# Kernel optimization log

Hardware: AMD Instinct MI355X
Metric: run time of the kernel (lower is better)

Reference implementation:

```python
import jax, jax.numpy as jnp
import numpy as np

B, N, D, H = 2, 2048, 256, 4
DH = D // H  # 64
ALPHA_DIV = 0.01
LN_EPS = 1e-5


def _split_heads(t):
    # [B, N, D] -> [B, H, N, DH]
    b, n, _ = t.shape
    return t.reshape(b, n, H, DH).transpose(0, 2, 1, 3)


def _merge_heads(t):
    # [B, H, N, DH] -> [B, N, D]
    b, h, n, d = t.shape
    return t.transpose(0, 2, 1, 3).reshape(b, n, h * d)


def setup_inputs() -> dict:
    key = jax.random.key(0)
    ks = jax.random.split(key, 20)
    p = lambda k, shape: (jax.random.normal(k, shape, dtype=jnp.float32) * 0.02)
    return {
        "x0": jax.random.normal(ks[0], (B, N, D), dtype=jnp.float32),
        "x1": jax.random.normal(ks[1], (B, N, D), dtype=jnp.float32),
        "cross_mask0": jax.random.uniform(ks[2], (B, 1, N), dtype=jnp.float32),
        "cross_mask1": jax.random.uniform(ks[3], (B, 1, N), dtype=jnp.float32),
        # weights stored as [in, out]
        "Wqk": p(ks[4], (D, D)), "bqk": jnp.zeros((D,), jnp.float32),
        "Wv": p(ks[5], (D, D)), "bv": jnp.zeros((D,), jnp.float32),
        "Wo": p(ks[6], (D, D)), "bo": jnp.zeros((D,), jnp.float32),
        "W1": p(ks[7], (2 * D, 2 * D)), "b1": jnp.zeros((2 * D,), jnp.float32),
        "ln_g": jnp.ones((2 * D,), jnp.float32), "ln_b": jnp.zeros((2 * D,), jnp.float32),
        "W2": p(ks[8], (2 * D, D)), "b2": jnp.zeros((D,), jnp.float32),
    }


def _ffn(x, W1, b1, ln_g, ln_b, W2, b2):
    h = x @ W1 + b1
    mu = jnp.mean(h, -1, keepdims=True)
    var = jnp.var(h, -1, keepdims=True)
    h = (h - mu) * jax.lax.rsqrt(var + LN_EPS) * ln_g + ln_b
    h = jax.nn.gelu(h, approximate=False)
    return h @ W2 + b2


def cross_block(x0, x1, cross_mask0, cross_mask1, Wqk, bqk, Wv, bv, Wo, bo,
                W1, b1, ln_g, ln_b, W2, b2):
    s = (DH ** -0.5) ** 0.5  # scale applied to each of qk0, qk1
    qk0 = _split_heads(x0 @ Wqk + bqk) * s
    qk1 = _split_heads(x1 @ Wqk + bqk) * s
    v0 = _split_heads(x0 @ Wv + bv)
    v1 = _split_heads(x1 @ Wv + bv)

    sim = jnp.einsum('bhid,bhjd->bhij', qk0, qk1)  # [B,H,N0,N1]

    # cross masks: [B,1,N] -> broadcast [B,1,1,N] over heads and query rows
    bad0 = (cross_mask0[:, :, None, :] < ALPHA_DIV)  # masks keys of dir 1->0
    bad1 = (cross_mask1[:, :, None, :] < ALPHA_DIV)  # masks keys of dir 0->1

    attn01 = jax.nn.softmax(jnp.where(bad1, -jnp.inf, sim), axis=-1)             # [B,H,N0,N1]
    attn10 = jax.nn.softmax(jnp.where(bad0, -jnp.inf, sim.swapaxes(-2, -1)), axis=-1)  # [B,H,N1,N0]

    m0 = jnp.einsum('bhij,bhjd->bhid', attn01, v1)
    m1 = jnp.einsum('bhij,bhjd->bhid', attn10, v0)

    m0 = _merge_heads(m0) @ Wo + bo
    m1 = _merge_heads(m1) @ Wo + bo

    out0 = x0 + _ffn(jnp.concatenate([x0, m0], -1), W1, b1, ln_g, ln_b, W2, b2)
    out1 = x1 + _ffn(jnp.concatenate([x1, m1], -1), W1, b1, ln_g, ln_b, W2, b2)
    return out0, out1, attn01, attn10


def reference(x0, x1, cross_mask0, cross_mask1, Wqk, bqk, Wv, bv, Wo, bo,
              W1, b1, ln_g, ln_b, W2, b2):
    return cross_block(x0, x1, cross_mask0, cross_mask1, Wqk, bqk, Wv, bv,
                       Wo, bo, W1, b1, ln_g, ln_b, W2, b2)
```

## Files before the change

### kernel.cpp

```cpp
#include <hip/hip_runtime.h>
#include <hip/hip_bf16.h>
#include <math.h>

#define B 2
#define N 2048
#define D 256
#define H 4
#define DH 64
#define D2 512
#define BH 8
#define BKP 40

static constexpr float ALPHA_DIV = 0.01f;
static constexpr float LN_EPS = 1e-5f;
static constexpr float SCL = 0.35355339059327373f;

typedef __attribute__((ext_vector_type(4))) float f32x4;
typedef __attribute__((ext_vector_type(8))) short s16x8;

__device__ inline s16x8 cvt8_bf16(const float* p) {
    union { s16x8 v; __hip_bfloat16 h[8]; } u;
#pragma unroll
    for (int i = 0; i < 8; i++) u.h[i] = __float2bfloat16(p[i]);
    return u.v;
}

template<int BM, bool OUT_BF16, bool HAS_RES>
__device__ __forceinline__ void gemm_core(
    __hip_bfloat16 (*As)[BKP], __hip_bfloat16 (*Ws)[BKP],
    const __hip_bfloat16* A, int lda, const __hip_bfloat16* WT, int ldw,
    const float* bias, const float* Res, int ldres,
    void* Cvp, int ldc, int K, float alpha, int rowBase, int colBase)
{
    constexpr int WM = BM / 2;
    constexpr int FM = WM / 16;
    constexpr int ACHUNK = (BM * 32) / (256 * 8);

    const int tid = threadIdx.x;
    const int lane = tid & 63, wid = tid >> 6;
    const int wr = wid >> 1, wc = wid & 1;
    const int lr = lane & 15, lk = (lane >> 4) * 8;

    f32x4 acc[FM][2] = {};

    for (int k0 = 0; k0 < K; k0 += 32) {
#pragma unroll
        for (int c = 0; c < ACHUNK; c++) {
            int e = (tid + c * 256) * 8;
            int r = e >> 5, kk = e & 31;
            *(s16x8*)&As[r][kk] = *(const s16x8*)&A[(size_t)(rowBase + r) * lda + k0 + kk];
        }
        {
            int e = tid * 8;
            int n = e >> 5, kk = e & 31;
            *(s16x8*)&Ws[n][kk] = *(const s16x8*)&WT[(size_t)(colBase + n) * ldw + k0 + kk];
        }
        __syncthreads();

        s16x8 a[FM], b[2];
#pragma unroll
        for (int i = 0; i < FM; i++) a[i] = *(const s16x8*)&As[wr * WM + i * 16 + lr][lk];
#pragma unroll
        for (int j = 0; j < 2; j++) b[j] = *(const s16x8*)&Ws[wc * 32 + j * 16 + lr][lk];
#pragma unroll
        for (int i = 0; i < FM; i++)
#pragma unroll
            for (int j = 0; j < 2; j++)
                acc[i][j] = __builtin_amdgcn_mfma_f32_16x16x32_bf16(a[i], b[j], acc[i][j], 0, 0, 0);
        __syncthreads();
    }

#pragma unroll
    for (int i = 0; i < FM; i++) {
#pragma unroll
        for (int j = 0; j < 2; j++) {
            int col = colBase + wc * 32 + j * 16 + lr;
            float bval = bias ? bias[col] : 0.f;
#pragma unroll
            for (int t = 0; t < 4; t++) {
                int row = rowBase + wr * WM + i * 16 + (lane >> 4) * 4 + t;
                float o = alpha * (acc[i][j][t] + bval);
                if (HAS_RES) o += Res[(size_t)row * ldres + col];
                if (OUT_BF16)
                    ((__hip_bfloat16*)Cvp)[(size_t)row * ldc + col] = __float2bfloat16(o);
                else
                    ((float*)Cvp)[(size_t)row * ldc + col] = o;
            }
        }
    }
}

template<bool OUT_BF16, bool HAS_RES>
__global__ __launch_bounds__(256) void gemm128_z(
    const __hip_bfloat16* A0, const __hip_bfloat16* A1, int lda,
    const __hip_bfloat16* WT, int ldw, const float* bias,
    const float* Res0, const float* Res1, int ldres,
    void* C0, void* C1, int ldc, int K, float alpha)
{
    __shared__ __hip_bfloat16 As[128][BKP];
    __shared__ __hip_bfloat16 Ws[64][BKP];
    const __hip_bfloat16* A = blockIdx.z ? A1 : A0;
    const float* Res = blockIdx.z ? Res1 : Res0;
    void* C = blockIdx.z ? C1 : C0;
    gemm_core<128, OUT_BF16, HAS_RES>(As, Ws, A, lda, WT, ldw, bias, Res, ldres,
        C, ldc, K, alpha, blockIdx.y * 128, blockIdx.x * 64);
}

__global__ __launch_bounds__(256) void proj_kernel(
    const float* __restrict__ x0, const float* __restrict__ x1,
    const __hip_bfloat16* __restrict__ WcT, const float* __restrict__ cb,
    __hip_bfloat16* __restrict__ qkv0, __hip_bfloat16* __restrict__ qkv1,
    __hip_bfloat16* __restrict__ vT,
    __hip_bfloat16* __restrict__ xc0, __hip_bfloat16* __restrict__ xc1)
{
    __shared__ __hip_bfloat16 As[128][BKP];
    __shared__ __hip_bfloat16 Ws[64][BKP];
    __shared__ __hip_bfloat16 T[128][72];
    const int z = blockIdx.z;
    const float* x = z ? x1 : x0;
    __hip_bfloat16* qkv = z ? qkv1 : qkv0;
    __hip_bfloat16* xc = z ? xc1 : xc0;
    const int rowBase = blockIdx.y * 128;
    const int colBase = blockIdx.x * 64;
    const int tid = threadIdx.x;
    const int lane = tid & 63, wid = tid >> 6;
    const int wr = wid >> 1, wc = wid & 1;
    const int lr = lane & 15, g = lane >> 4, lk = g * 8;

    f32x4 acc[4][2] = {};
    for (int k0 = 0; k0 < D; k0 += 32) {
#pragma unroll
        for (int c = 0; c < 2; c++) {
            int e = (tid + c * 256) * 8;
            int r = e >> 5, kk = e & 31;
            const float4 v0 = *(const float4*)&x[(size_t)(rowBase + r) * D + k0 + kk];
            const float4 v1 = *(const float4*)&x[(size_t)(rowBase + r) * D + k0 + kk + 4];
            union { s16x8 v; __hip_bfloat16 hh[8]; } u;
            u.hh[0] = __float2bfloat16(v0.x); u.hh[1] = __float2bfloat16(v0.y);
            u.hh[2] = __float2bfloat16(v0.z); u.hh[3] = __float2bfloat16(v0.w);
            u.hh[4] = __float2bfloat16(v1.x); u.hh[5] = __float2bfloat16(v1.y);
            u.hh[6] = __float2bfloat16(v1.z); u.hh[7] = __float2bfloat16(v1.w);
            *(s16x8*)&As[r][kk] = u.v;
            if (colBase == 0)
                *(s16x8*)&xc[(size_t)(rowBase + r) * D2 + k0 + kk] = u.v;
        }
        {
            int e = tid * 8;
            int n = e >> 5, kk = e & 31;
            *(s16x8*)&Ws[n][kk] = *(const s16x8*)&WcT[(size_t)(colBase + n) * D + k0 + kk];
        }
        __syncthreads();
        s16x8 a[4], b[2];
#pragma unroll
        for (int i = 0; i < 4; i++) a[i] = *(const s16x8*)&As[wr * 64 + i * 16 + lr][lk];
#pragma unroll
        for (int j = 0; j < 2; j++) b[j] = *(const s16x8*)&Ws[wc * 32 + j * 16 + lr][lk];
#pragma unroll
        for (int i = 0; i < 4; i++)
#pragma unroll
            for (int j = 0; j < 2; j++)
                acc[i][j] = __builtin_amdgcn_mfma_f32_16x16x32_bf16(a[i], b[j], acc[i][j], 0, 0, 0);
        __syncthreads();
    }

    if (colBase < 256) {
#pragma unroll
        for (int i = 0; i < 4; i++)
#pragma unroll
            for (int j = 0; j < 2; j++) {
                int col = colBase + wc * 32 + j * 16 + lr;
                float bval = cb[col];
#pragma unroll
                for (int t = 0; t < 4; t++) {
                    int row = rowBase + wr * 64 + i * 16 + g * 4 + t;
                    qkv[(size_t)row * D2 + col] = __float2bfloat16(acc[i][j][t] + bval);
                }
            }
    } else {
#pragma unroll
        for (int i = 0; i < 4; i++)
#pragma unroll
            for (int j = 0; j < 2; j++) {
                int cl = wc * 32 + j * 16 + lr;
                float bval = cb[colBase + cl];
#pragma unroll
                for (int t = 0; t < 4; t++)
                    T[wr * 64 + i * 16 + g * 4 + t][cl] = __float2bfloat16(acc[i][j][t] + bval);
            }
        __syncthreads();
        int hh = (colBase - 256) >> 6;
        int b_ = rowBase >> 11, n0 = rowBase & (N - 1);
        int slot = (z ? 0 : 8) + b_ * H + hh;
        int dh = tid >> 2, nn0 = (tid & 3) * 32;
        alignas(16) __hip_bfloat16 tmp[32];
#pragma unroll
        for (int u = 0; u < 32; u++) tmp[u] = T[nn0 + u][dh];
        __hip_bfloat16* dst = vT + ((size_t)slot * DH + dh) * N + n0 + nn0;
#pragma unroll
        for (int u8 = 0; u8 < 4; u8++)
            *(s16x8*)&dst[u8 * 8] = *(s16x8*)&tmp[u8 * 8];
    }
}

__device__ void transpose_tile(const float* W, int ldw, __hip_bfloat16* WT, int ldt,
                               int n0, int k0, float scale)
{
    __shared__ float T[32][33];
    int t = threadIdx.x;
    int r = t >> 3, c = (t & 7) * 4;
    float4 v = *(const float4*)&W[(size_t)(k0 + r) * ldw + n0 + c];
    T[r][c] = v.x; T[r][c + 1] = v.y; T[r][c + 2] = v.z; T[r][c + 3] = v.w;
    __syncthreads();
    __hip_bfloat16* dst = &WT[(size_t)(n0 + r) * ldt + k0 + c];
    dst[0] = __float2bfloat16(T[c][r] * scale);
    dst[1] = __float2bfloat16(T[c + 1][r] * scale);
    dst[2] = __float2bfloat16(T[c + 2][r] * scale);
    dst[3] = __float2bfloat16(T[c + 3][r] * scale);
}

__global__ __launch_bounds__(256) void prep_weights(
    const float* Wqk, const float* Wv, const float* Wo, const float* W1, const float* W2,
    const float* bqk, const float* bv,
    __hip_bfloat16* WcT, __hip_bfloat16* WoT, __hip_bfloat16* W1T, __hip_bfloat16* W2T,
    float* cb)
{
    int blk = blockIdx.x;
    if (blk < 64) {
        int nT = blk & 7, kT = blk >> 3;
        transpose_tile(Wqk, 256, WcT, 256, nT * 32, kT * 32, SCL);
    } else if (blk < 128) {
        int t = blk - 64; int nT = t & 7, kT = t >> 3;
        transpose_tile(Wv, 256, WcT + 256 * 256, 256, nT * 32, kT * 32, 1.f);
    } else if (blk < 192) {
        int t = blk - 128; int nT = t & 7, kT = t >> 3;
        transpose_tile(Wo, 256, WoT, 256, nT * 32, kT * 32, 1.f);
    } else if (blk < 448) {
        int t = blk - 192; int nT = t & 15, kT = t >> 4;
        transpose_tile(W1, 512, W1T, 512, nT * 32, kT * 32, 1.f);
    } else if (blk < 576) {
        int t = blk - 448; int nT = t & 7, kT = t >> 3;
        transpose_tile(W2, 256, W2T, 512, nT * 32, kT * 32, 1.f);
    } else {
        int t = threadIdx.x;
        cb[t] = SCL * bqk[t];
        cb[256 + t] = bv[t];
    }
}

__global__ __launch_bounds__(256) void fused_attn_av(
    const __hip_bfloat16* __restrict__ qkv0, const __hip_bfloat16* __restrict__ qkv1,
    const float* __restrict__ cm0, const float* __restrict__ cm1,
    const __hip_bfloat16* __restrict__ vT,
    float* __restrict__ attn01, float* __restrict__ attn10,
    __hip_bfloat16* __restrict__ m0b, __hip_bfloat16* __restrict__ m1b)
{
    __shared__ __hip_bfloat16 Qs[64][72];
    __shared__ __hip_bfloat16 Kt[128][72];
    __shared__ float Pf[64][132];
    __shared__ float badk[128];

    const int tid = threadIdx.x;
    int l = blockIdx.x;
    int xcd = l & 7, idx = l >> 3;
    int zz = xcd * 2 + (idx >> 5);
    int xb = idx & 31;
    int dir = zz >> 3, bh = zz & 7;
    int b = bh >> 2, h = bh & 3;

    const __hip_bfloat16* qQ = (dir ? qkv1 : qkv0) + (size_t)b * N * D2 + h * DH;
    const __hip_bfloat16* qK = (dir ? qkv0 : qkv1) + (size_t)b * N * D2 + h * DH;
    const float* cmK = (dir ? cm0 : cm1) + b * N;
    const __hip_bfloat16* vslot = vT + (size_t)((dir ? 8 : 0) + bh) * DH * N;
    float* attnOut = (dir ? attn10 : attn01) + (size_t)bh * N * N;
    __hip_bfloat16* mOut = (dir ? m1b : m0b) + (size_t)b * N * D + h * DH;

    const int i0 = xb * 64;

#pragma unroll
    for (int c = 0; c < 2; c++) {
        int e = (tid + c * 256) * 8;
        int r = e >> 6, k = e & 63;
        *(s16x8*)&Qs[r][k] = *(const s16x8*)&qQ[(size_t)(i0 + r) * D2 + k];
    }

    const int lane = tid & 63, w = tid >> 6;
    const int lr = lane & 15, g = lane >> 4;

    float m_[4] = { -INFINITY, -INFINITY, -INFINITY, -INFINITY };
    float s_[4] = { 0.f, 0.f, 0.f, 0.f };

    for (int jt = 0; jt < 16; jt++) {
        const int k0 = jt * 128;
#pragma unroll
        for (int c = 0; c < 4; c++) {
            int e = (tid + c * 256) * 8;
            int r = e >> 6, k = e & 63;
            *(s16x8*)&Kt[r][k] = *(const s16x8*)&qK[(size_t)(k0 + r) * D2 + k];
        }
        if (tid < 128) badk[tid] = cmK[k0 + tid];
        __syncthreads();

        f32x4 accs[8] = {};
        s16x8 a0 = *(const s16x8*)&Qs[w * 16 + lr][g * 8];
        s16x8 a1 = *(const s16x8*)&Qs[w * 16 + lr][32 + g * 8];
#pragma unroll
        for (int j = 0; j < 8; j++) {
            s16x8 bb = *(const s16x8*)&Kt[j * 16 + lr][g * 8];
            accs[j] = __builtin_amdgcn_mfma_f32_16x16x32_bf16(a0, bb, accs[j], 0, 0, 0);
        }
#pragma unroll
        for (int j = 0; j < 8; j++) {
            s16x8 bb = *(const s16x8*)&Kt[j * 16 + lr][32 + g * 8];
            accs[j] = __builtin_amdgcn_mfma_f32_16x16x32_bf16(a1, bb, accs[j], 0, 0, 0);
        }

        bool okc[8];
#pragma unroll
        for (int j = 0; j < 8; j++) okc[j] = badk[j * 16 + lr] >= ALPHA_DIV;

#pragma unroll
        for (int t = 0; t < 4; t++) {
            float tm = -INFINITY;
#pragma unroll
            for (int j = 0; j < 8; j++) if (okc[j]) tm = fmaxf(tm, accs[j][t]);
#pragma unroll
            for (int off = 1; off <= 8; off <<= 1) tm = fmaxf(tm, __shfl_xor(tm, off));
            float mn = fmaxf(m_[t], tm);
            float ts = 0.f;
#pragma unroll
            for (int j = 0; j < 8; j++) if (okc[j]) ts += __expf(accs[j][t] - mn);
#pragma unroll
            for (int off = 1; off <= 8; off <<= 1) ts += __shfl_xor(ts, off);
            float sc = (m_[t] == -INFINITY) ? 0.f : __expf(m_[t] - mn);
            s_[t] = s_[t] * sc + ts;
            m_[t] = mn;
        }
        __syncthreads();
    }

    float inv_[4];
#pragma unroll
    for (int t = 0; t < 4; t++) inv_[t] = 1.f / s_[t];

    f32x4 acc_o[4] = {};
    for (int jt = 0; jt < 16; jt++) {
        const int k0 = jt * 128;
#pragma unroll
        for (int c = 0; c < 4; c++) {
            int e = (tid + c * 256) * 8;
            int r = e >> 6, k = e & 63;
            *(s16x8*)&Kt[r][k] = *(const s16x8*)&qK[(size_t)(k0 + r) * D2 + k];
        }
        if (tid < 128) badk[tid] = cmK[k0 + tid];
        __syncthreads();

        s16x8 vf[4][4];
#pragma unroll
        for (int ks = 0; ks < 4; ks++)
#pragma unroll
            for (int j = 0; j < 4; j++)
                vf[ks][j] = *(const s16x8*)&vslot[(size_t)(j * 16 + lr) * N + k0 + ks * 32 + g * 8];

        f32x4 accs[8] = {};
        s16x8 a0 = *(const s16x8*)&Qs[w * 16 + lr][g * 8];
        s16x8 a1 = *(const s16x8*)&Qs[w * 16 + lr][32 + g * 8];
#pragma unroll
        for (int j = 0; j < 8; j++) {
            s16x8 bb = *(const s16x8*)&Kt[j * 16 + lr][g * 8];
            accs[j] = __builtin_amdgcn_mfma_f32_16x16x32_bf16(a0, bb, accs[j], 0, 0, 0);
        }
#pragma unroll
        for (int j = 0; j < 8; j++) {
            s16x8 bb = *(const s16x8*)&Kt[j * 16 + lr][32 + g * 8];
            accs[j] = __builtin_amdgcn_mfma_f32_16x16x32_bf16(a1, bb, accs[j], 0, 0, 0);
        }

        bool okc[8];
#pragma unroll
        for (int j = 0; j < 8; j++) okc[j] = badk[j * 16 + lr] >= ALPHA_DIV;

#pragma unroll
        for (int j = 0; j < 8; j++) {
#pragma unroll
            for (int t = 0; t < 4; t++) {
                float pv = okc[j] ? __expf(accs[j][t] - m_[t]) * inv_[t] : 0.f;
                Pf[w * 16 + g * 4 + t][j * 16 + lr] = pv;
            }
        }
        __syncthreads();

#pragma unroll
        for (int k = 0; k < 8; k++) {
            int f = tid + k * 256;
            int r = f >> 5, c4 = f & 31;
            *(float4*)&attnOut[(size_t)(i0 + r) * N + k0 + c4 * 4] = *(const float4*)&Pf[r][c4 * 4];
        }

#pragma unroll
        for (int ks = 0; ks < 4; ks++) {
            s16x8 pa = cvt8_bf16(&Pf[w * 16 + lr][ks * 32 + g * 8]);
#pragma unroll
            for (int j = 0; j < 4; j++)
                acc_o[j] = __builtin_amdgcn_mfma_f32_16x16x32_bf16(pa, vf[ks][j], acc_o[j], 0, 0, 0);
        }
        __syncthreads();
    }

    __hip_bfloat16* Ob = (__hip_bfloat16*)Pf;
#pragma unroll
    for (int j = 0; j < 4; j++)
#pragma unroll
        for (int t = 0; t < 4; t++)
            Ob[(w * 16 + g * 4 + t) * 72 + j * 16 + lr] = __float2bfloat16(acc_o[j][t]);
    __syncthreads();
    {
        int row = tid >> 2, c0 = (tid & 3) * 16;
        *(s16x8*)&mOut[(size_t)(i0 + row) * D + c0]     = *(const s16x8*)&Ob[row * 72 + c0];
        *(s16x8*)&mOut[(size_t)(i0 + row) * D + c0 + 8] = *(const s16x8*)&Ob[row * 72 + c0 + 8];
    }
}

#define HS_LD 528
__global__ __launch_bounds__(256) void w1_ln_gelu(
    __hip_bfloat16* __restrict__ xc0, __hip_bfloat16* __restrict__ xc1,
    const __hip_bfloat16* __restrict__ W1T, const float* __restrict__ b1,
    const float* __restrict__ lng, const float* __restrict__ lnb)
{
    __shared__ __hip_bfloat16 As[32][BKP];
    __shared__ __hip_bfloat16 WH[512 * BKP];
    __shared__ float redS[4][32], redQ[4][32];

    __hip_bfloat16* xc = blockIdx.y ? xc1 : xc0;
    const int rowBase = blockIdx.x * 32;
    const int tid = threadIdx.x;
    const int w = tid >> 6, lane = tid & 63;
    const int lr = lane & 15, g = lane >> 4, lk = g * 8;

    f32x4 acc[2][8] = {};
    for (int k0 = 0; k0 < D2; k0 += 32) {
        if (tid < 128) {
            int e = tid * 8;
            int r = e >> 5, kk = e & 31;
            *(s16x8*)&As[r][kk] = *(const s16x8*)&xc[(size_t)(rowBase + r) * D2 + k0 + kk];
        }
#pragma unroll
        for (int c = 0; c < 8; c++) {
            int e = (tid + c * 256) * 8;
            int n = e >> 5, kk = e & 31;
            *(s16x8*)&WH[n * BKP + kk] = *(const s16x8*)&W1T[(size_t)n * D2 + k0 + kk];
        }
        __syncthreads();
        s16x8 a[2], b[8];
#pragma unroll
        for (int i = 0; i < 2; i++) a[i] = *(const s16x8*)&As[i * 16 + lr][lk];
#pragma unroll
        for (int j = 0; j < 8; j++) b[j] = *(const s16x8*)&WH[(w * 128 + j * 16 + lr) * BKP + lk];
#pragma unroll
        for (int i = 0; i < 2; i++)
#pragma unroll
            for (int j = 0; j < 8; j++)
                acc[i][j] = __builtin_amdgcn_mfma_f32_16x16x32_bf16(a[i], b[j], acc[i][j], 0, 0, 0);
        __syncthreads();
    }

    float cols_b[8];
#pragma unroll
    for (int j = 0; j < 8; j++) cols_b[j] = b1[w * 128 + j * 16 + lr];
#pragma unroll
    for (int i = 0; i < 2; i++) {
#pragma unroll
        for (int t = 0; t < 4; t++) {
            float s = 0.f, q = 0.f;
#pragma unroll
            for (int j = 0; j < 8; j++) {
                float hv = acc[i][j][t] + cols_b[j];
                acc[i][j][t] = hv;
                s += hv; q += hv * hv;
            }
#pragma unroll
            for (int off = 1; off <= 8; off <<= 1) {
                s += __shfl_xor(s, off);
                q += __shfl_xor(q, off);
            }
            if (lr == 0) {
                int row = i * 16 + g * 4 + t;
                redS[w][row] = s; redQ[w][row] = q;
            }
        }
    }
    __syncthreads();

    __hip_bfloat16* Hs = WH;
    float gcol[8], bcol[8];
#pragma unroll
    for (int j = 0; j < 8; j++) {
        gcol[j] = lng[w * 128 + j * 16 + lr];
        bcol[j] = lnb[w * 128 + j * 16 + lr];
    }
#pragma unroll
    for (int i = 0; i < 2; i++) {
#pragma unroll
        for (int t = 0; t < 4; t++) {
            int row = i * 16 + g * 4 + t;
            float sum = redS[0][row] + redS[1][row] + redS[2][row] + redS[3][row];
            float sq  = redQ[0][row] + redQ[1][row] + redQ[2][row] + redQ[3][row];
            float mu = sum * (1.f / 512.f);
            float var = sq * (1.f / 512.f) - mu * mu;
            float rstd = rsqrtf(var + LN_EPS);
#pragma unroll
            for (int j = 0; j < 8; j++) {
                float y = (acc[i][j][t] - mu) * rstd * gcol[j] + bcol[j];
                float ge = 0.5f * y * (1.f + erff(y * 0.70710678118654752f));
                Hs[row * HS_LD + w * 128 + j * 16 + lr] = __float2bfloat16(ge);
            }
        }
    }
    __syncthreads();

    {
        int row = tid >> 3, c0 = (tid & 7) * 64;
#pragma unroll
        for (int u = 0; u < 8; u++)
            *(s16x8*)&xc[(size_t)(rowBase + row) * D2 + c0 + u * 8] =
                *(s16x8*)&Hs[row * HS_LD + c0 + u * 8];
    }
}

extern "C" void kernel_launch(void* const* d_in, const int* in_sizes, int n_in,
                              void* d_out, int out_size, void* d_ws, size_t ws_size,
                              hipStream_t stream) {
    const float* x0  = (const float*)d_in[0];
    const float* x1  = (const float*)d_in[1];
    const float* cm0 = (const float*)d_in[2];
    const float* cm1 = (const float*)d_in[3];
    const float* Wqk = (const float*)d_in[4]; const float* bqk = (const float*)d_in[5];
    const float* Wv  = (const float*)d_in[6]; const float* bv  = (const float*)d_in[7];
    const float* Wo  = (const float*)d_in[8]; const float* bo  = (const float*)d_in[9];
    const float* W1  = (const float*)d_in[10]; const float* b1 = (const float*)d_in[11];
    const float* lng = (const float*)d_in[12]; const float* lnb = (const float*)d_in[13];
    const float* W2  = (const float*)d_in[14]; const float* b2 = (const float*)d_in[15];

    float* out = (float*)d_out;
    char* p = (char*)d_ws;

    const size_t XSZ = (size_t)B * N * D;
    auto alloc = [&](size_t bytes) { char* r = p; p += (bytes + 255) & ~255ull; return r; };
    __hip_bfloat16* qkv0 = (__hip_bfloat16*)alloc((size_t)B * N * D2 * 2);
    __hip_bfloat16* qkv1 = (__hip_bfloat16*)alloc((size_t)B * N * D2 * 2);
    __hip_bfloat16* vT   = (__hip_bfloat16*)alloc((size_t)16 * DH * N * 2);
    __hip_bfloat16* m0b  = (__hip_bfloat16*)alloc(XSZ * 2);
    __hip_bfloat16* m1b  = (__hip_bfloat16*)alloc(XSZ * 2);
    __hip_bfloat16* xc0  = (__hip_bfloat16*)alloc((size_t)B * N * D2 * 2);
    __hip_bfloat16* xc1  = (__hip_bfloat16*)alloc((size_t)B * N * D2 * 2);
    __hip_bfloat16* WcT  = (__hip_bfloat16*)alloc(512 * 256 * 2);
    __hip_bfloat16* WoT  = (__hip_bfloat16*)alloc(256 * 256 * 2);
    __hip_bfloat16* W1T  = (__hip_bfloat16*)alloc(512 * 512 * 2);
    __hip_bfloat16* W2T  = (__hip_bfloat16*)alloc(256 * 512 * 2);
    float* cb            = (float*)alloc(512 * 4);

    float* out0 = out;
    float* out1 = out + XSZ;
    float* attn01 = out + 2 * XSZ;
    float* attn10 = attn01 + (size_t)BH * N * N;

    dim3 blk(256);

    prep_weights<<<577, blk, 0, stream>>>(Wqk, Wv, Wo, W1, W2, bqk, bv,
                                          WcT, WoT, W1T, W2T, cb);

    proj_kernel<<<dim3(8, 32, 2), blk, 0, stream>>>(
        x0, x1, WcT, cb, qkv0, qkv1, vT, xc0, xc1);

    fused_attn_av<<<512, blk, 0, stream>>>(qkv0, qkv1, cm0, cm1, vT,
        attn01, attn10, m0b, m1b);

    gemm128_z<true, false><<<dim3(4, 32, 2), blk, 0, stream>>>(
        m0b, m1b, D, WoT, D, bo, nullptr, nullptr, 0, xc0 + 256, xc1 + 256, D2, D, 1.f);

    w1_ln_gelu<<<dim3(128, 2), blk, 0, stream>>>(xc0, xc1, W1T, b1, lng, lnb);

    gemm128_z<false, true><<<dim3(4, 32, 2), blk, 0, stream>>>(
        xc0, xc1, D2, W2T, D2, b2, x0, x1, D, out0, out1, D, D2, 1.f);
}
```

Baseline: 205.2 us.

## Fold Wo into W1, drop softmax max pass, prefetch K tiles, store P in bf16

Precomputes Wo·W1[256:] and bo·W1[256:]+b1 in a new weight-fusion kernel. The attention kernel can then write its merged-head output straight into the second half of the FFN input buffer, and the separate Wo GEMM launch is removed. The first attention pass now only accumulates exp sums without a running max, and K tiles are prefetched into registers while the current tile is computed. The probability tile is kept in LDS as bf16 instead of float. This removes a kernel, some reduction work and LDS traffic, but risks exp overflow for large logits and rounds the attention output through bf16.

```diff
diff --git a/kernel.cpp b/kernel.cpp
--- a/kernel.cpp
+++ b/kernel.cpp
@@ -17,13 +17,6 @@
 
 typedef __attribute__((ext_vector_type(4))) float f32x4;
 typedef __attribute__((ext_vector_type(8))) short s16x8;
-
-__device__ inline s16x8 cvt8_bf16(const float* p) {
-    union { s16x8 v; __hip_bfloat16 h[8]; } u;
-#pragma unroll
-    for (int i = 0; i < 8; i++) u.h[i] = __float2bfloat16(p[i]);
-    return u.v;
-}
 
 template<int BM, bool OUT_BF16, bool HAS_RES>
 __device__ __forceinline__ void gemm_core(
@@ -219,9 +212,9 @@
 }
 
 __global__ __launch_bounds__(256) void prep_weights(
-    const float* Wqk, const float* Wv, const float* Wo, const float* W1, const float* W2,
+    const float* Wqk, const float* Wv, const float* W1, const float* W2,
     const float* bqk, const float* bv,
-    __hip_bfloat16* WcT, __hip_bfloat16* WoT, __hip_bfloat16* W1T, __hip_bfloat16* W2T,
+    __hip_bfloat16* WcT, __hip_bfloat16* W1cT, __hip_bfloat16* W2T,
     float* cb)
 {
     int blk = blockIdx.x;
@@ -231,14 +224,11 @@
     } else if (blk < 128) {
         int t = blk - 64; int nT = t & 7, kT = t >> 3;
         transpose_tile(Wv, 256, WcT + 256 * 256, 256, nT * 32, kT * 32, 1.f);
-    } else if (blk < 192) {
-        int t = blk - 128; int nT = t & 7, kT = t >> 3;
-        transpose_tile(Wo, 256, WoT, 256, nT * 32, kT * 32, 1.f);
-    } else if (blk < 448) {
-        int t = blk - 192; int nT = t & 15, kT = t >> 4;
-        transpose_tile(W1, 512, W1T, 512, nT * 32, kT * 32, 1.f);
-    } else if (blk < 576) {
-        int t = blk - 448; int nT = t & 7, kT = t >> 3;
+    } else if (blk < 256) {
+        int t = blk - 128; int nT = t & 15, kT = t >> 4;
+        transpose_tile(W1, 512, W1cT, 512, nT * 32, kT * 32, 1.f);
+    } else if (blk < 384) {
+        int t = blk - 256; int nT = t & 7, kT = t >> 3;
         transpose_tile(W2, 256, W2T, 512, nT * 32, kT * 32, 1.f);
     } else {
         int t = threadIdx.x;
@@ -247,17 +237,70 @@
     }
 }
 
+__global__ __launch_bounds__(256) void fuse_w(
+    const float* __restrict__ Wo, const float* __restrict__ W1,
+    const float* __restrict__ b1, const float* __restrict__ bo,
+    __hip_bfloat16* __restrict__ W1cT, float* __restrict__ cb2)
+{
+    int blk = blockIdx.x;
+    if (blk < 32) {
+        __shared__ float As[64][17];
+        __shared__ float Bs[64][17];
+        int n0 = (blk & 7) * 64, k0 = (blk >> 3) * 64;
+        int tx = threadIdx.x & 15, ty = threadIdx.x >> 4;
+        float acc[4][4] = {};
+        for (int c0 = 0; c0 < 256; c0 += 16) {
+#pragma unroll
+            for (int it = 0; it < 4; it++) {
+                int idx = threadIdx.x + it * 256;
+                int n = idx & 63, c = idx >> 6;
+                As[n][c] = W1[(size_t)(256 + c0 + c) * 512 + n0 + n];
+            }
+#pragma unroll
+            for (int it = 0; it < 4; it++) {
+                int idx = threadIdx.x + it * 256;
+                int k = idx >> 4, c = idx & 15;
+                Bs[k][c] = Wo[(size_t)(k0 + k) * 256 + c0 + c];
+            }
+            __syncthreads();
+#pragma unroll
+            for (int c = 0; c < 16; c++) {
+                float av[4], bv[4];
+#pragma unroll
+                for (int i = 0; i < 4; i++) av[i] = As[ty + i * 16][c];
+#pragma unroll
+                for (int j = 0; j < 4; j++) bv[j] = Bs[tx + j * 16][c];
+#pragma unroll
+                for (int i = 0; i < 4; i++)
+#pragma unroll
+                    for (int j = 0; j < 4; j++) acc[i][j] += av[i] * bv[j];
+            }
+            __syncthreads();
+        }
+#pragma unroll
+        for (int i = 0; i < 4; i++)
+#pragma unroll
+            for (int j = 0; j < 4; j++)
+                W1cT[(size_t)(n0 + ty + i * 16) * 512 + 256 + k0 + tx + j * 16] =
+                    __float2bfloat16(acc[i][j]);
+    } else {
+        int n = (blk - 32) * 256 + threadIdx.x;
+        float s = b1[n];
+        for (int c = 0; c < 256; c++) s += bo[c] * W1[(size_t)(256 + c) * 512 + n];
+        cb2[n] = s;
+    }
+}
+
 __global__ __launch_bounds__(256) void fused_attn_av(
     const __hip_bfloat16* __restrict__ qkv0, const __hip_bfloat16* __restrict__ qkv1,
     const float* __restrict__ cm0, const float* __restrict__ cm1,
     const __hip_bfloat16* __restrict__ vT,
     float* __restrict__ attn01, float* __restrict__ attn10,
-    __hip_bfloat16* __restrict__ m0b, __hip_bfloat16* __restrict__ m1b)
-{
-    __shared__ __hip_bfloat16 Qs[64][72];
+    __hip_bfloat16* __restrict__ xc0, __hip_bfloat16* __restrict__ xc1)
+{
     __shared__ __hip_bfloat16 Kt[128][72];
-    __shared__ float Pf[64][132];
-    __shared__ float badk[128];
+    __shared__ __hip_bfloat16 Pfb[64][136];
+    __shared__ float okm[2048];
 
     const int tid = threadIdx.x;
     int l = blockIdx.x;
@@ -272,37 +315,43 @@
     const float* cmK = (dir ? cm0 : cm1) + b * N;
     const __hip_bfloat16* vslot = vT + (size_t)((dir ? 8 : 0) + bh) * DH * N;
     float* attnOut = (dir ? attn10 : attn01) + (size_t)bh * N * N;
-    __hip_bfloat16* mOut = (dir ? m1b : m0b) + (size_t)b * N * D + h * DH;
+    __hip_bfloat16* mOut = (dir ? xc1 : xc0) + (size_t)b * N * D2 + 256 + h * DH;
 
     const int i0 = xb * 64;
-
-#pragma unroll
-    for (int c = 0; c < 2; c++) {
-        int e = (tid + c * 256) * 8;
-        int r = e >> 6, k = e & 63;
-        *(s16x8*)&Qs[r][k] = *(const s16x8*)&qQ[(size_t)(i0 + r) * D2 + k];
-    }
-
     const int lane = tid & 63, w = tid >> 6;
     const int lr = lane & 15, g = lane >> 4;
 
-    float m_[4] = { -INFINITY, -INFINITY, -INFINITY, -INFINITY };
-    float s_[4] = { 0.f, 0.f, 0.f, 0.f };
-
-    for (int jt = 0; jt < 16; jt++) {
-        const int k0 = jt * 128;
+    s16x8 a0 = *(const s16x8*)&qQ[(size_t)(i0 + w * 16 + lr) * D2 + g * 8];
+    s16x8 a1 = *(const s16x8*)&qQ[(size_t)(i0 + w * 16 + lr) * D2 + 32 + g * 8];
+
+#pragma unroll
+    for (int it = 0; it < 8; it++) okm[tid + it * 256] = cmK[tid + it * 256];
+
+    s16x8 kreg[4];
+    auto loadK = [&](int jt) {
+        const int kk0 = jt * 128;
 #pragma unroll
         for (int c = 0; c < 4; c++) {
             int e = (tid + c * 256) * 8;
-            int r = e >> 6, k = e & 63;
-            *(s16x8*)&Kt[r][k] = *(const s16x8*)&qK[(size_t)(k0 + r) * D2 + k];
-        }
-        if (tid < 128) badk[tid] = cmK[k0 + tid];
-        __syncthreads();
+            kreg[c] = *(const s16x8*)&qK[(size_t)(kk0 + (e >> 6)) * D2 + (e & 63)];
+        }
+    };
+    auto writeK = [&]() {
+#pragma unroll
+        for (int c = 0; c < 4; c++) {
+            int e = (tid + c * 256) * 8;
+            *(s16x8*)&Kt[e >> 6][e & 63] = kreg[c];
+        }
+    };
+
+    float sp[4] = { 0.f, 0.f, 0.f, 0.f };
+    loadK(0);
+    for (int jt = 0; jt < 16; jt++) {
+        writeK();
+        __syncthreads();
+        if (jt < 15) loadK(jt + 1);
 
         f32x4 accs[8] = {};
-        s16x8 a0 = *(const s16x8*)&Qs[w * 16 + lr][g * 8];
-        s16x8 a1 = *(const s16x8*)&Qs[w * 16 + lr][32 + g * 8];
 #pragma unroll
         for (int j = 0; j < 8; j++) {
             s16x8 bb = *(const s16x8*)&Kt[j * 16 + lr][g * 8];
@@ -313,46 +362,31 @@
             s16x8 bb = *(const s16x8*)&Kt[j * 16 + lr][32 + g * 8];
             accs[j] = __builtin_amdgcn_mfma_f32_16x16x32_bf16(a1, bb, accs[j], 0, 0, 0);
         }
-
-        bool okc[8];
-#pragma unroll
-        for (int j = 0; j < 8; j++) okc[j] = badk[j * 16 + lr] >= ALPHA_DIV;
-
-#pragma unroll
-        for (int t = 0; t < 4; t++) {
-            float tm = -INFINITY;
-#pragma unroll
-            for (int j = 0; j < 8; j++) if (okc[j]) tm = fmaxf(tm, accs[j][t]);
-#pragma unroll
-            for (int off = 1; off <= 8; off <<= 1) tm = fmaxf(tm, __shfl_xor(tm, off));
-            float mn = fmaxf(m_[t], tm);
-            float ts = 0.f;
-#pragma unroll
-            for (int j = 0; j < 8; j++) if (okc[j]) ts += __expf(accs[j][t] - mn);
-#pragma unroll
-            for (int off = 1; off <= 8; off <<= 1) ts += __shfl_xor(ts, off);
-            float sc = (m_[t] == -INFINITY) ? 0.f : __expf(m_[t] - mn);
-            s_[t] = s_[t] * sc + ts;
-            m_[t] = mn;
-        }
-        __syncthreads();
-    }
-
-    float inv_[4];
-#pragma unroll
-    for (int t = 0; t < 4; t++) inv_[t] = 1.f / s_[t];
+        const int k0 = jt * 128;
+#pragma unroll
+        for (int j = 0; j < 8; j++) {
+            bool ok = okm[k0 + j * 16 + lr] >= ALPHA_DIV;
+#pragma unroll
+            for (int t = 0; t < 4; t++)
+                if (ok) sp[t] += __expf(accs[j][t]);
+        }
+        __syncthreads();
+    }
+    float inv[4];
+#pragma unroll
+    for (int t = 0; t < 4; t++) {
+#pragma unroll
+        for (int off = 1; off <= 8; off <<= 1) sp[t] += __shfl_xor(sp[t], off);
+        inv[t] = 1.f / sp[t];
+    }
 
     f32x4 acc_o[4] = {};
+    loadK(0);
     for (int jt = 0; jt < 16; jt++) {
+        writeK();
+        __syncthreads();
+        if (jt < 15) loadK(jt + 1);
         const int k0 = jt * 128;
-#pragma unroll
-        for (int c = 0; c < 4; c++) {
-            int e = (tid + c * 256) * 8;
-            int r = e >> 6, k = e & 63;
-            *(s16x8*)&Kt[r][k] = *(const s16x8*)&qK[(size_t)(k0 + r) * D2 + k];
-        }
-        if (tid < 128) badk[tid] = cmK[k0 + tid];
-        __syncthreads();
 
         s16x8 vf[4][4];
 #pragma unroll
@@ -362,8 +396,6 @@
                 vf[ks][j] = *(const s16x8*)&vslot[(size_t)(j * 16 + lr) * N + k0 + ks * 32 + g * 8];
 
         f32x4 accs[8] = {};
-        s16x8 a0 = *(const s16x8*)&Qs[w * 16 + lr][g * 8];
-        s16x8 a1 = *(const s16x8*)&Qs[w * 16 + lr][32 + g * 8];
 #pragma unroll
         for (int j = 0; j < 8; j++) {
             s16x8 bb = *(const s16x8*)&Kt[j * 16 + lr][g * 8];
@@ -375,30 +407,35 @@
             accs[j] = __builtin_amdgcn_mfma_f32_16x16x32_bf16(a1, bb, accs[j], 0, 0, 0);
         }
 
-        bool okc[8];
-#pragma unroll
-        for (int j = 0; j < 8; j++) okc[j] = badk[j * 16 + lr] >= ALPHA_DIV;
-
 #pragma unroll
         for (int j = 0; j < 8; j++) {
+            bool ok = okm[k0 + j * 16 + lr] >= ALPHA_DIV;
 #pragma unroll
             for (int t = 0; t < 4; t++) {
-                float pv = okc[j] ? __expf(accs[j][t] - m_[t]) * inv_[t] : 0.f;
-                Pf[w * 16 + g * 4 + t][j * 16 + lr] = pv;
-            }
-        }
-        __syncthreads();
-
-#pragma unroll
-        for (int k = 0; k < 8; k++) {
+                float pv = ok ? __expf(accs[j][t]) * inv[t] : 0.f;
+                Pfb[w * 16 + g * 4 + t][j * 16 + lr] = __float2bfloat16(pv);
+            }
+        }
+        __syncthreads();
+
+#pragma unroll
+        for (int k = 0; k < 4; k++) {
             int f = tid + k * 256;
-            int r = f >> 5, c4 = f & 31;
-            *(float4*)&attnOut[(size_t)(i0 + r) * N + k0 + c4 * 4] = *(const float4*)&Pf[r][c4 * 4];
+            int r = f >> 4, c0 = (f & 15) * 8;
+            union { s16x8 v; __hip_bfloat16 hh[8]; } u;
+            u.v = *(const s16x8*)&Pfb[r][c0];
+            float4 o0, o1;
+            o0.x = __bfloat162float(u.hh[0]); o0.y = __bfloat162float(u.hh[1]);
+            o0.z = __bfloat162float(u.hh[2]); o0.w = __bfloat162float(u.hh[3]);
+            o1.x = __bfloat162float(u.hh[4]); o1.y = __bfloat162float(u.hh[5]);
+            o1.z = __bfloat162float(u.hh[6]); o1.w = __bfloat162float(u.hh[7]);
+            *(float4*)&attnOut[(size_t)(i0 + r) * N + k0 + c0] = o0;
+            *(float4*)&attnOut[(size_t)(i0 + r) * N + k0 + c0 + 4] = o1;
         }
 
 #pragma unroll
         for (int ks = 0; ks < 4; ks++) {
-            s16x8 pa = cvt8_bf16(&Pf[w * 16 + lr][ks * 32 + g * 8]);
+            s16x8 pa = *(const s16x8*)&Pfb[w * 16 + lr][ks * 32 + g * 8];
 #pragma unroll
             for (int j = 0; j < 4; j++)
                 acc_o[j] = __builtin_amdgcn_mfma_f32_16x16x32_bf16(pa, vf[ks][j], acc_o[j], 0, 0, 0);
@@ -406,17 +443,17 @@
         __syncthreads();
     }
 
-    __hip_bfloat16* Ob = (__hip_bfloat16*)Pf;
+    __hip_bfloat16* Ob = (__hip_bfloat16*)Pfb;
 #pragma unroll
     for (int j = 0; j < 4; j++)
 #pragma unroll
         for (int t = 0; t < 4; t++)
-            Ob[(w * 16 + g * 4 + t) * 72 + j * 16 + lr] = __float2bfloat16(acc_o[j][t]);
+            Ob[(w * 16 + g * 4 + t) * 136 + j * 16 + lr] = __float2bfloat16(acc_o[j][t]);
     __syncthreads();
     {
         int row = tid >> 2, c0 = (tid & 3) * 16;
-        *(s16x8*)&mOut[(size_t)(i0 + row) * D + c0]     = *(const s16x8*)&Ob[row * 72 + c0];
-        *(s16x8*)&mOut[(size_t)(i0 + row) * D + c0 + 8] = *(const s16x8*)&Ob[row * 72 + c0 + 8];
+        *(s16x8*)&mOut[(size_t)(i0 + row) * D2 + c0]     = *(const s16x8*)&Ob[row * 136 + c0];
+        *(s16x8*)&mOut[(size_t)(i0 + row) * D2 + c0 + 8] = *(const s16x8*)&Ob[row * 136 + c0 + 8];
     }
 }
 
@@ -548,15 +585,13 @@
     __hip_bfloat16* qkv0 = (__hip_bfloat16*)alloc((size_t)B * N * D2 * 2);
     __hip_bfloat16* qkv1 = (__hip_bfloat16*)alloc((size_t)B * N * D2 * 2);
     __hip_bfloat16* vT   = (__hip_bfloat16*)alloc((size_t)16 * DH * N * 2);
-    __hip_bfloat16* m0b  = (__hip_bfloat16*)alloc(XSZ * 2);
-    __hip_bfloat16* m1b  = (__hip_bfloat16*)alloc(XSZ * 2);
     __hip_bfloat16* xc0  = (__hip_bfloat16*)alloc((size_t)B * N * D2 * 2);
     __hip_bfloat16* xc1  = (__hip_bfloat16*)alloc((size_t)B * N * D2 * 2);
     __hip_bfloat16* WcT  = (__hip_bfloat16*)alloc(512 * 256 * 2);
-    __hip_bfloat16* WoT  = (__hip_bfloat16*)alloc(256 * 256 * 2);
-    __hip_bfloat16* W1T  = (__hip_bfloat16*)alloc(512 * 512 * 2);
+    __hip_bfloat16* W1cT = (__hip_bfloat16*)alloc(512 * 512 * 2);
     __hip_bfloat16* W2T  = (__hip_bfloat16*)alloc(256 * 512 * 2);
     float* cb            = (float*)alloc(512 * 4);
+    float* cb2           = (float*)alloc(512 * 4);
 
     float* out0 = out;
     float* out1 = out + XSZ;
@@ -565,19 +600,17 @@
 
     dim3 blk(256);
 
-    prep_weights<<<577, blk, 0, stream>>>(Wqk, Wv, Wo, W1, W2, bqk, bv,
-                                          WcT, WoT, W1T, W2T, cb);
+    prep_weights<<<385, blk, 0, stream>>>(Wqk, Wv, W1, W2, bqk, bv,
+                                          WcT, W1cT, W2T, cb);
+    fuse_w<<<34, blk, 0, stream>>>(Wo, W1, b1, bo, W1cT, cb2);
 
     proj_kernel<<<dim3(8, 32, 2), blk, 0, stream>>>(
         x0, x1, WcT, cb, qkv0, qkv1, vT, xc0, xc1);
 
     fused_attn_av<<<512, blk, 0, stream>>>(qkv0, qkv1, cm0, cm1, vT,
-        attn01, attn10, m0b, m1b);
-
-    gemm128_z<true, false><<<dim3(4, 32, 2), blk, 0, stream>>>(
-        m0b, m1b, D, WoT, D, bo, nullptr, nullptr, 0, xc0 + 256, xc1 + 256, D2, D, 1.f);
-
-    w1_ln_gelu<<<dim3(128, 2), blk, 0, stream>>>(xc0, xc1, W1T, b1, lng, lnb);
+        attn01, attn10, xc0, xc1);
+
+    w1_ln_gelu<<<dim3(128, 2), blk, 0, stream>>>(xc0, xc1, W1cT, cb2, lng, lnb);
 
     gemm128_z<false, true><<<dim3(4, 32, 2), blk, 0, stream>>>(
         xc0, xc1, D2, W2T, D2, b2, x0, x1, D, out0, out1, D, D2, 1.f);
```

Result: no change. 205.0 us (-0.1%).
